# Optimization experiments

Hardware: AMD Instinct MI355X
Metric: run time of the kernel (lower is better)

Reference implementation:

```python
import jax, jax.numpy as jnp
import numpy as np
import math

B, L, D, H = 4, 2048, 1024, 16
HD = D // H


def setup_inputs() -> dict:
    key = jax.random.key(0)
    k1, k2, k3 = jax.random.split(key, 3)
    x = jax.random.normal(k1, (B, L, D), dtype=jnp.float32)
    # Linear weights stored as [in, out] so y = x @ W (equivalent to torch x @ W.T)
    Wqkv = jax.random.normal(k2, (D, 3 * D), dtype=jnp.float32) * (1.0 / math.sqrt(D))
    Wproj = jax.random.normal(k3, (D, D), dtype=jnp.float32) * (1.0 / math.sqrt(D))
    attn_mask = jnp.tril(jnp.ones((L, L), dtype=bool))  # True = attend (causal)
    key_padding_mask = jnp.zeros((B, L), dtype=bool)     # True = padded (none here)
    return {"x": x, "Wqkv": Wqkv, "Wproj": Wproj,
            "attn_mask": attn_mask, "key_padding_mask": key_padding_mask}


def reference(x, Wqkv, Wproj, attn_mask, key_padding_mask):
    Bx, Lx, Dx = x.shape
    qkv = x @ Wqkv                              # [B, L, 3D]
    q, k, v = jnp.split(qkv, 3, axis=-1)
    def shape(t):
        return t.reshape(Bx, Lx, H, HD).transpose(0, 2, 1, 3)  # [B, H, L, hd]
    q, k, v = shape(q), shape(k), shape(v)
    att = jnp.einsum('bhqd,bhkd->bhqk', q, k) / math.sqrt(HD)  # [B, H, L, L]
    neg_inf = jnp.float32(-jnp.inf)
    att = jnp.where(attn_mask[None, None, :, :], att, neg_inf)
    att = jnp.where(key_padding_mask[:, None, None, :], neg_inf, att)
    att = jax.nn.softmax(att, axis=-1)
    y = jnp.einsum('bhqk,bhkd->bhqd', att, v)   # [B, H, L, hd]
    y = y.transpose(0, 2, 1, 3).reshape(Bx, Lx, Dx)
    return y @ Wproj
```

## Files before the change

kernel.cpp:

```cpp
#include <hip/hip_runtime.h>
#include <cstdint>
#include <cstddef>


typedef __attribute__((ext_vector_type(8))) __bf16 bf16x8;
typedef __attribute__((ext_vector_type(4))) __bf16 bf16x4;
typedef __attribute__((ext_vector_type(4))) float f32x4;
typedef __attribute__((ext_vector_type(16))) float f32x16;

__device__ __forceinline__ f32x4 mfma_bf16(bf16x8 a, bf16x8 b, f32x4 c) {
  return __builtin_amdgcn_mfma_f32_16x16x32_bf16(a, b, c, 0, 0, 0);
}

__device__ __forceinline__ f32x16 mfma32(bf16x8 a, bf16x8 b, f32x16 c) {
  return __builtin_amdgcn_mfma_f32_32x32x16_bf16(a, b, c, 0, 0, 0);
}

__device__ __forceinline__ unsigned cvtpk(float a, float b) {
  unsigned r;
  asm("v_cvt_pk_bf16_f32 %0, %1, %2" : "=v"(r) : "v"(a), "v"(b));
  return r;
}

__device__ __forceinline__ void async_copy16(const void* gsrc, void* ldsdst) {
  __builtin_amdgcn_global_load_lds(
      (const __attribute__((address_space(1))) void*)gsrc,
      (__attribute__((address_space(3))) void*)ldsdst, 16, 0, 0);
}

__global__ __launch_bounds__(256) void prep(
    const float* __restrict__ x, __bf16* __restrict__ xb,
    const float* __restrict__ Wqkv, __bf16* __restrict__ WqkvT,
    const float* __restrict__ Wproj, __bf16* __restrict__ WprojT) {
  const int bid = blockIdx.x;
  if (bid < 8192) {
    const size_t i = ((size_t)bid * 256 + threadIdx.x) * 4;
    const float4 v = *(const float4*)&x[i];
    bf16x4 o = {(__bf16)v.x, (__bf16)v.y, (__bf16)v.z, (__bf16)v.w};
    *(bf16x4*)&xb[i] = o;
    return;
  }
  __shared__ float tile[32][33];
  const float* in;
  __bf16* out;
  int idx, gx, R, C;
  if (bid < 8192 + 3072) {
    idx = bid - 8192; in = Wqkv; out = WqkvT; R = 1024; C = 3072; gx = 96;
  } else {
    idx = bid - 11264; in = Wproj; out = WprojT; R = 1024; C = 1024; gx = 32;
  }
  const int c0 = (idx % gx) * 32;
  const int r0 = (idx / gx) * 32;
  const int tx = threadIdx.x & 31;
  const int ty = threadIdx.x >> 5;
#pragma unroll
  for (int i = 0; i < 32; i += 8)
    tile[ty + i][tx] = in[(size_t)(r0 + ty + i) * C + c0 + tx];
  __syncthreads();
#pragma unroll
  for (int i = 0; i < 32; i += 8)
    out[(size_t)(c0 + ty + i) * R + r0 + tx] = (__bf16)tile[tx][ty + i];
}

#define GEMM128x128_CORE(Aptr, Bptr)                                         \
  const int srow32 = tid >> 3;                                    \
  const int schunk = ((tid & 7) ^ (srow32 & 7)) << 3;                        \
  const __bf16* aBase = &(Aptr)[(size_t)(m0 + srow32) * 1024 + schunk];      \
  const __bf16* bBase = &(Bptr)[(size_t)(n0 + srow32) * 1024 + schunk];      \
  auto stgTile = [&](int kt, int b2) {                                       \
    __bf16* dst = smem + b2 * 16384 + wave * 512;                            \
    _Pragma("unroll") for (int u = 0; u < 4; ++u)                            \
        async_copy16(aBase + (size_t)u * 32768 + kt * 64, dst + u * 2048);   \
    _Pragma("unroll") for (int u = 0; u < 4; ++u)                            \
        async_copy16(bBase + (size_t)u * 32768 + kt * 64,                    \
                     dst + 8192 + u * 2048);                                 \
  };                                                                         \
  const f32x4 zero = {0.f, 0.f, 0.f, 0.f};                                   \
  f32x4 acc[4][4];                                                           \
  _Pragma("unroll") for (int i = 0; i < 4; ++i)                              \
      _Pragma("unroll") for (int j = 0; j < 4; ++j) acc[i][j] = zero;        \
  stgTile(0, 0);                                                             \
  asm volatile("s_waitcnt vmcnt(0)" ::: "memory");                           \
  __builtin_amdgcn_s_barrier();                                              \
  for (int t = 0; t < 16; ++t) {                                             \
    const __bf16* As = smem + (t & 1) * 16384;                               \
    const __bf16* Bs = As + 8192;                                            \
    bf16x8 af[4][2], bfr[4][2];                                              \
    _Pragma("unroll") for (int mt = 0; mt < 4; ++mt)                         \
        _Pragma("unroll") for (int kk = 0; kk < 2; ++kk) af[mt][kk] =        \
            *(const bf16x8*)&As[(wr * 64 + mt * 16 + n16) * 64 +             \
                                (((kk * 4 + quad) ^ (n16 & 7)) << 3)];       \
    _Pragma("unroll") for (int nt = 0; nt < 4; ++nt)                         \
        _Pragma("unroll") for (int kk = 0; kk < 2; ++kk) bfr[nt][kk] =       \
            *(const bf16x8*)&Bs[(wc * 64 + nt * 16 + n16) * 64 +             \
                                (((kk * 4 + quad) ^ (n16 & 7)) << 3)];       \
    if (t < 15) stgTile(t + 1, (t + 1) & 1);                                 \
    __builtin_amdgcn_s_barrier();                                            \
    asm volatile("s_waitcnt lgkmcnt(0)" ::: "memory");                       \
    __builtin_amdgcn_sched_barrier(0);                                       \
    __builtin_amdgcn_s_setprio(1);                                           \
    _Pragma("unroll") for (int mt = 0; mt < 4; ++mt)                         \
        _Pragma("unroll") for (int nt = 0; nt < 4; ++nt)                     \
            _Pragma("unroll") for (int kk = 0; kk < 2; ++kk)                 \
                acc[mt][nt] = mfma_bf16(af[mt][kk], bfr[nt][kk],             \
                                        acc[mt][nt]);                        \
    __builtin_amdgcn_s_setprio(0);                                           \
    asm volatile("s_waitcnt vmcnt(0)" ::: "memory");                         \
    __builtin_amdgcn_s_barrier();                                            \
  }

__global__ __launch_bounds__(256, 2) void gemm_qkv(
    const __bf16* __restrict__ A, const __bf16* __restrict__ BT,
    __bf16* __restrict__ Q, __bf16* __restrict__ Kh, __bf16* __restrict__ VT) {
  extern __shared__ __bf16 smem[];
  const int wg = (blockIdx.x & 7) * 192 + (blockIdx.x >> 3);
  const int bm = wg / 24;
  const int bn = wg % 24;
  const int m0 = bm << 7;
  const int n0 = bn << 7;
  const int tid = threadIdx.x;
  const int wave = tid >> 6;
  const int lane = tid & 63;
  const int n16 = lane & 15;
  const int quad = lane >> 4;
  const int wr = wave >> 1;
  const int wc = wave & 1;

  GEMM128x128_CORE(A, BT)

  __bf16* tw = smem + wave * 2048;
  const int b = m0 >> 11;
  const int l0w = (m0 & 2047) + wr * 64;
  const int n = n0 + wc * 64;

  if (n < 2048) {
    const float QSCALE = 0.125f * 1.44269504089f;
    const bool isQ = (n < 1024);
    const int h = (n & 1023) >> 6;
    __bf16* dst = isQ ? Q : Kh;
    const size_t base = ((size_t)(b * 16 + h) * 2048) * 64;
#pragma unroll
    for (int pass = 0; pass < 2; ++pass) {
#pragma unroll
      for (int mt = 2 * pass; mt < 2 * pass + 2; ++mt) {
#pragma unroll
        for (int nt = 0; nt < 4; ++nt)
#pragma unroll
          for (int r = 0; r < 4; ++r) {
            const int hd = nt * 16 + n16;
            const int mm = (mt & 1) * 16 + quad * 4 + r;
            const float v = isQ ? acc[mt][nt][r] * QSCALE : acc[mt][nt][r];
            tw[mm * 64 + (((hd >> 3) ^ (mm & 7)) << 3) + (hd & 7)] =
                (__bf16)v;
          }
      }
#pragma unroll
      for (int i = 0; i < 4; ++i) {
        const int c = lane + 64 * i;
        const int row = c >> 3;
        const int hd0 = (c & 7) << 3;
        const int phys = (c & 7) ^ (row & 7);
        const bf16x8 v = *(const bf16x8*)&tw[row * 64 + phys * 8];
        *(bf16x8*)&dst[base + (size_t)(l0w + pass * 32 + row) * 64 + hd0] = v;
      }
    }
  } else {
    const int h = (n - 2048) >> 6;
    const size_t bhead = (size_t)(b * 16 + h);
#pragma unroll
    for (int pass = 0; pass < 2; ++pass) {
#pragma unroll
      for (int nt = 2 * pass; nt < 2 * pass + 2; ++nt) {
#pragma unroll
        for (int mt = 0; mt < 4; ++mt)
#pragma unroll
          for (int r = 0; r < 4; ++r) {
            const int hdp = (nt & 1) * 16 + n16;
            const int mm = mt * 16 + quad * 4 + r;
            const int phys = (mm >> 3) ^ (hdp & 7);
            tw[hdp * 64 + phys * 8 + (mm & 7)] = (__bf16)acc[mt][nt][r];
          }
      }
#pragma unroll
      for (int i = 0; i < 4; ++i) {
        const int c = lane + 64 * i;
        const int row = c >> 3;
        const int phys = (c & 7) ^ (row & 7);
        const bf16x8 v = *(const bf16x8*)&tw[row * 64 + phys * 8];
        *(bf16x8*)&VT[(bhead * 64 + pass * 32 + row) * 2048 + l0w +
                      (c & 7) * 8] = v;
      }
    }
  }
}

__global__ __launch_bounds__(256, 2) void gemm_bt_f32out(
    const __bf16* __restrict__ A, const __bf16* __restrict__ BT,
    float* __restrict__ C) {
  extern __shared__ __bf16 smem[];
  const int wg = (blockIdx.x & 7) * 64 + (blockIdx.x >> 3);
  const int bm = wg >> 3;
  const int bn = wg & 7;
  const int m0 = bm << 7;
  const int n0 = bn << 7;
  const int tid = threadIdx.x;
  const int wave = tid >> 6;
  const int lane = tid & 63;
  const int n16 = lane & 15;
  const int quad = lane >> 4;
  const int wr = wave >> 1;
  const int wc = wave & 1;

  GEMM128x128_CORE(A, BT)

#pragma unroll
  for (int mt = 0; mt < 4; ++mt) {
#pragma unroll
    for (int r = 0; r < 4; ++r) {
      const int m = m0 + wr * 64 + mt * 16 + quad * 4 + r;
#pragma unroll
      for (int nt = 0; nt < 4; ++nt) {
        const int nn = n0 + wc * 64 + nt * 16 + n16;
        C[(size_t)m * 1024 + nn] = acc[mt][nt][r];
      }
    }
  }
}

__global__ __launch_bounds__(256, 2) void flash_attn(
    const __bf16* __restrict__ Q, const __bf16* __restrict__ Kh,
    const __bf16* __restrict__ VT, __bf16* __restrict__ Y) {
  __shared__ __bf16 Ks[4][64 * 64];
  __shared__ __bf16 Vs[4][64 * 64];
  const int bh = blockIdx.x;
  const int p = blockIdx.y;
  const int tid = threadIdx.x;
  const int wave = tid >> 6;
  const int lane = tid & 63;
  const int lrow = lane & 31;
  const int hi = lane >> 5;
  const int lswz = lane & 7;
  const __bf16* Qb = Q + (size_t)bh * 2048 * 64;
  const __bf16* Kb = Kh + (size_t)bh * 2048 * 64;
  const __bf16* Vb = VT + (size_t)bh * 64 * 2048;
  const int b = bh >> 4;
  const int h = bh & 15;
  const f32x16 zero16 = {0.f, 0.f, 0.f, 0.f, 0.f, 0.f, 0.f, 0.f,
                         0.f, 0.f, 0.f, 0.f, 0.f, 0.f, 0.f, 0.f};

  const int srow = tid >> 3;
  const int sswz = ((tid & 7) ^ (srow & 7)) << 3;
  const size_t kg0 = (size_t)srow * 64 + sswz;
  const size_t kg1 = (size_t)(srow + 32) * 64 + sswz;
  const size_t vg0 = (size_t)srow * 2048 + sswz;
  const size_t vg1 = (size_t)(srow + 32) * 2048 + sswz;
  const int ldst0 = wave * 512;
  const int ldst1 = 2048 + wave * 512;

  auto stage = [&](int cn, int b4) {
    async_copy16(&Kb[kg0 + (size_t)cn * 64], &Ks[b4][ldst0]);
    async_copy16(&Kb[kg1 + (size_t)cn * 64], &Ks[b4][ldst1]);
    async_copy16(&Vb[vg0 + cn], &Vs[b4][ldst0]);
    async_copy16(&Vb[vg1 + cn], &Vs[b4][ldst1]);
  };

#pragma unroll
  for (int tt = 0; tt < 2; ++tt) {
    const int t = tt ? 15 - p : p;
    const int q0w = t * 128 + wave * 32;
    const int myq = q0w + lrow;

    bf16x8 qf[4];
#pragma unroll
    for (int i = 0; i < 4; ++i)
      qf[i] = *(const bf16x8*)&Qb[(size_t)myq * 64 + i * 16 + hi * 8];

    f32x16 o0 = zero16, o1 = zero16;
    float lsum = 0.f;
    const int nsteps = 2 * (t + 1);

    __builtin_amdgcn_s_barrier();
    stage(0, 0);
    stage(64, 1);
    asm volatile("s_waitcnt vmcnt(4)" ::: "memory");
    __builtin_amdgcn_s_barrier();

    for (int kt = 0; kt < nsteps; ++kt) {
      const int c0 = kt << 6;
      const bool more = (kt + 2 < nsteps);
      if (more) stage((kt + 2) << 6, (kt + 2) & 3);

      if (c0 <= q0w + 31) {
        const __bf16* ks = Ks[kt & 3];
        const __bf16* vs = Vs[kt & 3];

        f32x16 sc[2];
#pragma unroll
        for (int ch = 0; ch < 2; ++ch) {
          sc[ch] = zero16;
#pragma unroll
          for (int i = 0; i < 4; ++i) {
            const bf16x8 kf = *(const bf16x8*)&ks[(ch * 32 + lrow) * 64 +
                                                  (((2 * i + hi) ^ lswz)
                                                   << 3)];
            sc[ch] = mfma32(kf, qf[i], sc[ch]);
          }
        }
        if (c0 + 63 > q0w) {
#pragma unroll
          for (int ch = 0; ch < 2; ++ch)
#pragma unroll
            for (int r = 0; r < 16; ++r) {
              const int k = c0 + ch * 32 + (r & 3) + 8 * (r >> 2) + 4 * hi;
              float e = __builtin_amdgcn_exp2f(sc[ch][r]);
              e = (k <= myq) ? e : 0.f;
              sc[ch][r] = e;
              lsum += e;
            }
        } else {
#pragma unroll
          for (int ch = 0; ch < 2; ++ch)
#pragma unroll
            for (int r = 0; r < 16; ++r) {
              const float e = __builtin_amdgcn_exp2f(sc[ch][r]);
              sc[ch][r] = e;
              lsum += e;
            }
        }
#pragma unroll
        for (int ch = 0; ch < 2; ++ch) {
#pragma unroll
          for (int kc = 0; kc < 2; ++kc) {
            unsigned c01 = cvtpk(sc[ch][kc * 8 + 0], sc[ch][kc * 8 + 1]);
            unsigned c23 = cvtpk(sc[ch][kc * 8 + 2], sc[ch][kc * 8 + 3]);
            unsigned c45 = cvtpk(sc[ch][kc * 8 + 4], sc[ch][kc * 8 + 5]);
            unsigned c67 = cvtpk(sc[ch][kc * 8 + 6], sc[ch][kc * 8 + 7]);
            asm("v_permlane32_swap_b32 %0, %1" : "+v"(c01), "+v"(c45));
            asm("v_permlane32_swap_b32 %0, %1" : "+v"(c23), "+v"(c67));
            union {
              unsigned u[4];
              bf16x8 v;
            } pu;
            pu.u[0] = c01;
            pu.u[1] = c23;
            pu.u[2] = c45;
            pu.u[3] = c67;
            const int kch = ch * 4 + kc * 2 + hi;
            {
              const bf16x8 vf0 = *(const bf16x8*)&vs[(0 * 32 + lrow) * 64 +
                                                     ((kch ^ lswz) << 3)];
              o0 = mfma32(pu.v, vf0, o0);
              const bf16x8 vf1 = *(const bf16x8*)&vs[(1 * 32 + lrow) * 64 +
                                                     ((kch ^ lswz) << 3)];
              o1 = mfma32(pu.v, vf1, o1);
            }
          }
        }
      }

      if (kt + 1 < nsteps) {
        if (more)
          asm volatile("s_waitcnt vmcnt(4)" ::: "memory");
        else
          asm volatile("s_waitcnt vmcnt(0)" ::: "memory");
        __builtin_amdgcn_s_barrier();
      }
    }

    lsum += __shfl_xor(lsum, 32);
    const float inv = 1.0f / lsum;
    float invr[16];
#pragma unroll
    for (int r = 0; r < 16; ++r)
      invr[r] = __shfl(inv, (r & 3) + 8 * (r >> 2) + 4 * hi);
#pragma unroll
    for (int r = 0; r < 16; ++r) {
      const int row = q0w + (r & 3) + 8 * (r >> 2) + 4 * hi;
      const size_t yb = (size_t)(b * 2048 + row) * 1024 + h * 64;
      Y[yb + lrow] = (__bf16)(o0[r] * invr[r]);
      Y[yb + 32 + lrow] = (__bf16)(o1[r] * invr[r]);
    }
  }
}

extern "C" void kernel_launch(void* const* d_in, const int* in_sizes, int n_in,
                              void* d_out, int out_size, void* d_ws,
                              size_t ws_size, hipStream_t stream) {
  const float* x = (const float*)d_in[0];
  const float* Wqkv = (const float*)d_in[1];
  const float* Wproj = (const float*)d_in[2];
  float* out = (float*)d_out;

  char* ws = (char*)d_ws;
  __bf16* xb = (__bf16*)ws;     ws += (size_t)8192 * 1024 * 2;
  __bf16* WqkvT = (__bf16*)ws;  ws += (size_t)3072 * 1024 * 2;
  __bf16* WprojT = (__bf16*)ws; ws += (size_t)1024 * 1024 * 2;
  __bf16* Qs = (__bf16*)ws;     ws += (size_t)64 * 2048 * 64 * 2;
  __bf16* Ks = (__bf16*)ws;     ws += (size_t)64 * 2048 * 64 * 2;
  __bf16* VTs = (__bf16*)ws;    ws += (size_t)64 * 64 * 2048 * 2;
  __bf16* attn = xb;

  static bool attrSet = false;
  if (!attrSet) {
    hipFuncSetAttribute((const void*)gemm_qkv,
                        hipFuncAttributeMaxDynamicSharedMemorySize, 65536);
    hipFuncSetAttribute((const void*)gemm_bt_f32out,
                        hipFuncAttributeMaxDynamicSharedMemorySize, 65536);
    attrSet = true;
  }

  prep<<<12288, 256, 0, stream>>>(x, xb, Wqkv, WqkvT, Wproj, WprojT);
  gemm_qkv<<<1536, 256, 65536, stream>>>(xb, WqkvT, Qs, Ks, VTs);
  flash_attn<<<dim3(64, 8), 256, 0, stream>>>(Qs, Ks, VTs, attn);
  gemm_bt_f32out<<<512, 256, 65536, stream>>>(attn, WprojT, out);
}
```

Baseline: 233.2 us.

## Split paired causal tiles into separate blocks and compute row sums via MFMA

Each block previously handled two query tiles (t and 15-t) to balance causal work. Now one block handles one tile on a 64x16 grid, with three LDS stages instead of four and launch bounds raised to three blocks per CU. The softmax denominator is now built by an extra MFMA of the probabilities against a ones vector, replacing the scalar lsum accumulation and shuffles. Per-block work is now unbalanced across tiles, and the extra MFMA per chunk adds matrix-unit load and uses bf16-rounded probabilities in the sum.

Measured after the change: 239.5 us. 1.03x slower.

```diff
diff --git a/kernel.cpp b/kernel.cpp
--- a/kernel.cpp
+++ b/kernel.cpp
@@ -227,13 +227,13 @@
   }
 }
 
-__global__ __launch_bounds__(256, 2) void flash_attn(
+__global__ __launch_bounds__(256, 3) void flash_attn(
     const __bf16* __restrict__ Q, const __bf16* __restrict__ Kh,
     const __bf16* __restrict__ VT, __bf16* __restrict__ Y) {
-  __shared__ __bf16 Ks[4][64 * 64];
-  __shared__ __bf16 Vs[4][64 * 64];
+  __shared__ __bf16 Ks[3][64 * 64];
+  __shared__ __bf16 Vs[3][64 * 64];
   const int bh = blockIdx.x;
-  const int p = blockIdx.y;
+  const int t = blockIdx.y;
   const int tid = threadIdx.x;
   const int wave = tid >> 6;
   const int lane = tid & 63;
@@ -247,6 +247,13 @@
   const int h = bh & 15;
   const f32x16 zero16 = {0.f, 0.f, 0.f, 0.f, 0.f, 0.f, 0.f, 0.f,
                          0.f, 0.f, 0.f, 0.f, 0.f, 0.f, 0.f, 0.f};
+  union {
+    unsigned short u[8];
+    bf16x8 v;
+  } onesu;
+#pragma unroll
+  for (int i = 0; i < 8; ++i) onesu.u[i] = 0x3F80;
+  const bf16x8 onesf = onesu.v;
 
   const int srow = tid >> 3;
   const int sswz = ((tid & 7) ^ (srow & 7)) << 3;
@@ -257,129 +264,111 @@
   const int ldst0 = wave * 512;
   const int ldst1 = 2048 + wave * 512;
 
-  auto stage = [&](int cn, int b4) {
-    async_copy16(&Kb[kg0 + (size_t)cn * 64], &Ks[b4][ldst0]);
-    async_copy16(&Kb[kg1 + (size_t)cn * 64], &Ks[b4][ldst1]);
-    async_copy16(&Vb[vg0 + cn], &Vs[b4][ldst0]);
-    async_copy16(&Vb[vg1 + cn], &Vs[b4][ldst1]);
+  auto stage = [&](int cn, int b3) {
+    async_copy16(&Kb[kg0 + (size_t)cn * 64], &Ks[b3][ldst0]);
+    async_copy16(&Kb[kg1 + (size_t)cn * 64], &Ks[b3][ldst1]);
+    async_copy16(&Vb[vg0 + cn], &Vs[b3][ldst0]);
+    async_copy16(&Vb[vg1 + cn], &Vs[b3][ldst1]);
   };
 
-#pragma unroll
-  for (int tt = 0; tt < 2; ++tt) {
-    const int t = tt ? 15 - p : p;
-    const int q0w = t * 128 + wave * 32;
-    const int myq = q0w + lrow;
-
-    bf16x8 qf[4];
-#pragma unroll
-    for (int i = 0; i < 4; ++i)
-      qf[i] = *(const bf16x8*)&Qb[(size_t)myq * 64 + i * 16 + hi * 8];
-
-    f32x16 o0 = zero16, o1 = zero16;
-    float lsum = 0.f;
-    const int nsteps = 2 * (t + 1);
-
-    __builtin_amdgcn_s_barrier();
-    stage(0, 0);
-    stage(64, 1);
-    asm volatile("s_waitcnt vmcnt(4)" ::: "memory");
-    __builtin_amdgcn_s_barrier();
-
-    for (int kt = 0; kt < nsteps; ++kt) {
-      const int c0 = kt << 6;
-      const bool more = (kt + 2 < nsteps);
-      if (more) stage((kt + 2) << 6, (kt + 2) & 3);
-
-      if (c0 <= q0w + 31) {
-        const __bf16* ks = Ks[kt & 3];
-        const __bf16* vs = Vs[kt & 3];
-
-        f32x16 sc[2];
-#pragma unroll
-        for (int ch = 0; ch < 2; ++ch) {
-          sc[ch] = zero16;
-#pragma unroll
-          for (int i = 0; i < 4; ++i) {
-            const bf16x8 kf = *(const bf16x8*)&ks[(ch * 32 + lrow) * 64 +
-                                                  (((2 * i + hi) ^ lswz)
-                                                   << 3)];
-            sc[ch] = mfma32(kf, qf[i], sc[ch]);
+  const int q0w = t * 128 + wave * 32;
+  const int myq = q0w + lrow;
+
+  bf16x8 qf[4];
+#pragma unroll
+  for (int i = 0; i < 4; ++i)
+    qf[i] = *(const bf16x8*)&Qb[(size_t)myq * 64 + i * 16 + hi * 8];
+
+  f32x16 o0 = zero16, o1 = zero16, os = zero16;
+  const int nsteps = 2 * (t + 1);
+
+  stage(0, 0);
+  stage(64, 1);
+  asm volatile("s_waitcnt vmcnt(4)" ::: "memory");
+  __builtin_amdgcn_s_barrier();
+
+  for (int kt = 0; kt < nsteps; ++kt) {
+    const int c0 = kt << 6;
+    const bool more = (kt + 2 < nsteps);
+    if (more) stage((kt + 2) << 6, (kt + 2) % 3);
+
+    if (c0 <= q0w + 31) {
+      const __bf16* ks = Ks[kt % 3];
+      const __bf16* vs = Vs[kt % 3];
+
+      f32x16 sc[2];
+#pragma unroll
+      for (int ch = 0; ch < 2; ++ch) {
+        sc[ch] = zero16;
+#pragma unroll
+        for (int i = 0; i < 4; ++i) {
+          const bf16x8 kf = *(const bf16x8*)&ks[(ch * 32 + lrow) * 64 +
+                                                (((2 * i + hi) ^ lswz) << 3)];
+          sc[ch] = mfma32(kf, qf[i], sc[ch]);
+        }
+      }
+      if (c0 + 63 > q0w) {
+#pragma unroll
+        for (int ch = 0; ch < 2; ++ch)
+#pragma unroll
+          for (int r = 0; r < 16; ++r) {
+            const int k = c0 + ch * 32 + (r & 3) + 8 * (r >> 2) + 4 * hi;
+            float e = __builtin_amdgcn_exp2f(sc[ch][r]);
+            sc[ch][r] = (k <= myq) ? e : 0.f;
           }
+      } else {
+#pragma unroll
+        for (int ch = 0; ch < 2; ++ch)
+#pragma unroll
+          for (int r = 0; r < 16; ++r)
+            sc[ch][r] = __builtin_amdgcn_exp2f(sc[ch][r]);
+      }
+#pragma unroll
+      for (int ch = 0; ch < 2; ++ch) {
+#pragma unroll
+        for (int kc = 0; kc < 2; ++kc) {
+          unsigned c01 = cvtpk(sc[ch][kc * 8 + 0], sc[ch][kc * 8 + 1]);
+          unsigned c23 = cvtpk(sc[ch][kc * 8 + 2], sc[ch][kc * 8 + 3]);
+          unsigned c45 = cvtpk(sc[ch][kc * 8 + 4], sc[ch][kc * 8 + 5]);
+          unsigned c67 = cvtpk(sc[ch][kc * 8 + 6], sc[ch][kc * 8 + 7]);
+          asm("v_permlane32_swap_b32 %0, %1" : "+v"(c01), "+v"(c45));
+          asm("v_permlane32_swap_b32 %0, %1" : "+v"(c23), "+v"(c67));
+          union {
+            unsigned u[4];
+            bf16x8 v;
+          } pu;
+          pu.u[0] = c01;
+          pu.u[1] = c23;
+          pu.u[2] = c45;
+          pu.u[3] = c67;
+          const int kch = ch * 4 + kc * 2 + hi;
+          const bf16x8 vf0 = *(const bf16x8*)&vs[(0 * 32 + lrow) * 64 +
+                                                 ((kch ^ lswz) << 3)];
+          o0 = mfma32(pu.v, vf0, o0);
+          const bf16x8 vf1 = *(const bf16x8*)&vs[(1 * 32 + lrow) * 64 +
+                                                 ((kch ^ lswz) << 3)];
+          o1 = mfma32(pu.v, vf1, o1);
+          os = mfma32(pu.v, onesf, os);
         }
-        if (c0 + 63 > q0w) {
-#pragma unroll
-          for (int ch = 0; ch < 2; ++ch)
-#pragma unroll
-            for (int r = 0; r < 16; ++r) {
-              const int k = c0 + ch * 32 + (r & 3) + 8 * (r >> 2) + 4 * hi;
-              float e = __builtin_amdgcn_exp2f(sc[ch][r]);
-              e = (k <= myq) ? e : 0.f;
-              sc[ch][r] = e;
-              lsum += e;
-            }
-        } else {
-#pragma unroll
-          for (int ch = 0; ch < 2; ++ch)
-#pragma unroll
-            for (int r = 0; r < 16; ++r) {
-              const float e = __builtin_amdgcn_exp2f(sc[ch][r]);
-              sc[ch][r] = e;
-              lsum += e;
-            }
-        }
-#pragma unroll
-        for (int ch = 0; ch < 2; ++ch) {
-#pragma unroll
-          for (int kc = 0; kc < 2; ++kc) {
-            unsigned c01 = cvtpk(sc[ch][kc * 8 + 0], sc[ch][kc * 8 + 1]);
-            unsigned c23 = cvtpk(sc[ch][kc * 8 + 2], sc[ch][kc * 8 + 3]);
-            unsigned c45 = cvtpk(sc[ch][kc * 8 + 4], sc[ch][kc * 8 + 5]);
-            unsigned c67 = cvtpk(sc[ch][kc * 8 + 6], sc[ch][kc * 8 + 7]);
-            asm("v_permlane32_swap_b32 %0, %1" : "+v"(c01), "+v"(c45));
-            asm("v_permlane32_swap_b32 %0, %1" : "+v"(c23), "+v"(c67));
-            union {
-              unsigned u[4];
-              bf16x8 v;
-            } pu;
-            pu.u[0] = c01;
-            pu.u[1] = c23;
-            pu.u[2] = c45;
-            pu.u[3] = c67;
-            const int kch = ch * 4 + kc * 2 + hi;
-            {
-              const bf16x8 vf0 = *(const bf16x8*)&vs[(0 * 32 + lrow) * 64 +
-                                                     ((kch ^ lswz) << 3)];
-              o0 = mfma32(pu.v, vf0, o0);
-              const bf16x8 vf1 = *(const bf16x8*)&vs[(1 * 32 + lrow) * 64 +
-                                                     ((kch ^ lswz) << 3)];
-              o1 = mfma32(pu.v, vf1, o1);
-            }
-          }
-        }
-      }
-
-      if (kt + 1 < nsteps) {
-        if (more)
-          asm volatile("s_waitcnt vmcnt(4)" ::: "memory");
-        else
-          asm volatile("s_waitcnt vmcnt(0)" ::: "memory");
-        __builtin_amdgcn_s_barrier();
       }
     }
 
-    lsum += __shfl_xor(lsum, 32);
-    const float inv = 1.0f / lsum;
-    float invr[16];
-#pragma unroll
-    for (int r = 0; r < 16; ++r)
-      invr[r] = __shfl(inv, (r & 3) + 8 * (r >> 2) + 4 * hi);
-#pragma unroll
-    for (int r = 0; r < 16; ++r) {
-      const int row = q0w + (r & 3) + 8 * (r >> 2) + 4 * hi;
-      const size_t yb = (size_t)(b * 2048 + row) * 1024 + h * 64;
-      Y[yb + lrow] = (__bf16)(o0[r] * invr[r]);
-      Y[yb + 32 + lrow] = (__bf16)(o1[r] * invr[r]);
+    if (kt + 1 < nsteps) {
+      if (more)
+        asm volatile("s_waitcnt vmcnt(4)" ::: "memory");
+      else
+        asm volatile("s_waitcnt vmcnt(0)" ::: "memory");
+      __builtin_amdgcn_s_barrier();
     }
+  }
+
+#pragma unroll
+  for (int r = 0; r < 16; ++r) {
+    const float inv = 1.0f / os[r];
+    const int row = q0w + (r & 3) + 8 * (r >> 2) + 4 * hi;
+    const size_t yb = (size_t)(b * 2048 + row) * 1024 + h * 64;
+    Y[yb + lrow] = (__bf16)(o0[r] * inv);
+    Y[yb + 32 + lrow] = (__bf16)(o1[r] * inv);
   }
 }
 
@@ -411,6 +400,6 @@
 
   prep<<<12288, 256, 0, stream>>>(x, xb, Wqkv, WqkvT, Wproj, WprojT);
   gemm_qkv<<<1536, 256, 65536, stream>>>(xb, WqkvT, Qs, Ks, VTs);
-  flash_attn<<<dim3(64, 8), 256, 0, stream>>>(Qs, Ks, VTs, attn);
+  flash_attn<<<dim3(64, 16), 256, 0, stream>>>(Qs, Ks, VTs, attn);
   gemm_bt_f32out<<<512, 256, 65536, stream>>>(attn, WprojT, out);
 }
```
